# Optimization experiments

Hardware: AMD Instinct MI355X
Metric: run time of the kernel (lower is better)

The kernel has to match this reference:

```python
import jax, jax.numpy as jnp
import numpy as np
import math

LMAX = 3
NCHAN = 32
NEDGE = 50000

# ---------- Wigner 3j (real spherical-harmonic basis), replicating e3nn ----------

def _su2_cg(j1, j2, j3):
    f = math.factorial
    def coeff(m1, m2, m3):
        vmin = int(max(-j1 + j2 + m3, -j1 + m1, 0))
        vmax = int(min(j2 + j3 + m1, j3 - j1 + j2, j3 + m3))
        C = ((2 * j3 + 1) * f(j3 + j1 - j2) * f(j3 - j1 + j2) * f(j1 + j2 - j3) / f(j1 + j2 + j3 + 1)) ** 0.5
        C *= (f(j3 + m3) * f(j3 - m3) * f(j1 - m1) * f(j1 + m1) * f(j2 - m2) * f(j2 + m2)) ** 0.5
        S = 0.0
        for v in range(vmin, vmax + 1):
            S += (-1.0) ** (v + j2 + m2) * f(j2 + j3 + m1 - v) * f(j1 - m1 + v) / (
                f(v) * f(j3 - j1 + j2 - v) * f(j3 + m3 - v) * f(v + j1 - j2 - m3))
        return C * S
    out = np.zeros((2 * j1 + 1, 2 * j2 + 1, 2 * j3 + 1))
    for m1 in range(-j1, j1 + 1):
        for m2 in range(-j2, j2 + 1):
            m3 = m1 + m2
            if -j3 <= m3 <= j3:
                out[m1 + j1, m2 + j2, m3 + j3] = coeff(m1, m2, m3)
    return out

def _q_real_to_complex(l):
    q = np.zeros((2 * l + 1, 2 * l + 1), dtype=np.complex128)
    for m in range(-l, 0):
        q[l + m, l + abs(m)] = 1 / 2 ** 0.5
        q[l + m, l - abs(m)] = -1j / 2 ** 0.5
    q[l, l] = 1.0
    for m in range(1, l + 1):
        q[l + m, l + abs(m)] = (-1) ** m / 2 ** 0.5
        q[l + m, l - abs(m)] = 1j * (-1) ** m / 2 ** 0.5
    return (-1j) ** l * q

def _wigner_3j(l1, l2, l3):
    C = _su2_cg(l1, l2, l3).astype(np.complex128)
    Q1, Q2, Q3 = _q_real_to_complex(l1), _q_real_to_complex(l2), _q_real_to_complex(l3)
    C = np.einsum('ij,kl,mn,ikn->jlm', Q1, Q2, np.conj(Q3.T), C)
    C = np.real(C)
    return C / np.linalg.norm(C)

# ---------- Instruction enumeration (matches the torch module's __init__) ----------

def _build_paths():
    ls = list(range(LMAX + 1))  # irreps 0e,1o,2e,3o -> parity (-1)^l
    ins = []
    for l1 in ls:
        for l2 in ls:
            for l3 in range(abs(l1 - l2), min(l1 + l2, LMAX) + 1):
                if (l1 + l2 + l3) % 2 == 0:  # parity selection p1*p2 == p3
                    ins.append((l1, l2, l3))
    # e3nn Irreps.sort: stable sort of output blocks by ir; pos[i] = sorted position
    order_sorted = sorted(range(len(ins)), key=lambda i: ins[i][2])
    pos = [0] * len(ins)
    for new, old in enumerate(order_sorted):
        pos[old] = new
    # replicate `outputs.insert(ins.i_out, output)` over instruction iteration order
    concat = []
    for idx in range(len(ins)):
        concat.insert(min(pos[idx], len(concat)), idx)
    offs = np.cumsum([0] + [2 * l + 1 for l in ls]).tolist()  # block offsets in dim-16 layout
    # path_weight: component normalization, one path per output block -> sqrt(2*l3+1)
    cg = [jnp.asarray((_wigner_3j(l1, l2, l3) * math.sqrt(2 * l3 + 1)).astype(np.float32))
          for (l1, l2, l3) in ins]
    return ins, pos, concat, offs, cg

_INS, _POS, _CONCAT, _OFFS, _CG = _build_paths()  # 23 instructions, out dim 99


def setup_inputs() -> dict:
    key = jax.random.key(0)
    k1, k2, k3 = jax.random.split(key, 3)
    x = jax.random.normal(k1, (NEDGE, NCHAN, 16), dtype=jnp.float32)
    y = jax.random.normal(k2, (NEDGE, 1, 16), dtype=jnp.float32)
    weights = jax.random.normal(k3, (NEDGE, len(_INS) * NCHAN, 1), dtype=jnp.float32)
    return {"x": x, "y": y, "weights": weights}


def reference(x, y, weights):
    # x: [E, C, 16], y: [E, 1, 16], weights: [E, n_ins*C, 1]
    C = x.shape[1]
    y2 = y[:, 0, :]  # [E, 16]
    outs = [None] * len(_INS)
    for idx, (l1, l2, l3) in enumerate(_INS):
        o1, o2 = _OFFS[l1], _OFFS[l2]
        xb = x[:, :, o1:o1 + 2 * l1 + 1]            # [E, C, 2l1+1]
        yb = y2[:, o2:o2 + 2 * l2 + 1]              # [E, 2l2+1]
        w = weights[:, _POS[idx] * C:(_POS[idx] + 1) * C, 0]  # [E, C]
        # dense CG contraction == sparse gather-multiply-index_add over (mu1,mu2,mu3)
        blk = jnp.einsum('eci,ej,ijk->eck', xb, yb, _CG[idx])  # [E, C, 2l3+1]
        outs[idx] = w[:, :, None] * blk
    return jnp.concatenate([outs[i] for i in _CONCAT], axis=-1)  # [E, C, 99]
```

## Files before the change

kernel.cpp:

```cpp
#include <hip/hip_runtime.h>
#include <math.h>

#define NPATH 23
#define NEDGE 50000
#define NCHAN 32
#define NWROW 736
#define OUTW  99
#define TTOT  439
#define EPB   4
#define NTHR  512
#define NBLK  (NEDGE/EPB)

constexpr int L1[NPATH]    = {0,0,0,0,1,1,1,1,1,1,2,2,2,2,2,2,2,3,3,3,3,3,3};
constexpr int L2[NPATH]    = {0,1,2,3,0,1,1,2,2,3,0,1,1,2,2,3,3,0,1,2,2,3,3};
constexpr int L3[NPATH]    = {0,1,2,3,1,0,2,1,3,2,2,1,3,0,2,1,3,3,2,1,3,0,2};
constexpr int POS[NPATH]   = {0,4,10,17,5,1,11,6,18,12,13,7,19,2,14,8,20,21,15,9,22,3,16};
constexpr int OOFF[NPATH]  = {0,4,7,12,19,1,34,22,39,46,51,31,61,2,73,25,78,85,68,28,92,3,56};
constexpr int TOFF[NPATH]  = {0,1,4,9,16,25,28,43,52,73,88,113,128,163,168,193,208,243,292,327,348,397,404};
constexpr int LOFF[4]      = {0,1,4,9};

#define G0M  0xE0010u
#define G1M  0x700100u
#define G2M  0x7C00u
#define G3LO 0x2Fu
#define G3HI 0x182C0u

typedef _Float16 __attribute__((ext_vector_type(4))) h4;

__device__ __forceinline__ int imx(int a, int b){ return a > b ? a : b; }
__device__ __forceinline__ int imn(int a, int b){ return a < b ? a : b; }

__device__ __forceinline__ double factd(int n){
    double r = 1.0;
    for(int i = 2; i <= n; ++i) r *= (double)i;
    return r;
}

__global__ __launch_bounds__(512) void cg_setup(float* __restrict__ cgd2){
    const int p  = blockIdx.x;
    const int j1 = L1[p], j2 = L2[p], j3 = L3[p];
    const int n1 = 2*j1+1, n2 = 2*j2+1, n3 = 2*j3+1;
    const int o2 = LOFF[j2];
    const int ntot = n1*n2*n3;
    const int t = threadIdx.x;

    __shared__ double scg[343];
    __shared__ double qre[3][49];
    __shared__ double qim[3][49];
    __shared__ double red[512];

    if(t < ntot){
        int a   = t / (n2*n3);
        int rem = t - a*(n2*n3);
        int b   = rem / n3;
        int g   = rem - b*n3;
        int m1 = a - j1, m2 = b - j2, m3 = g - j3;
        double val = 0.0;
        if(m1 + m2 == m3){
            int vmin = imx(imx(-j1 + j2 + m3, -j1 + m1), 0);
            int vmax = imn(imn(j2 + j3 + m1, j3 - j1 + j2), j3 + m3);
            double C = sqrt((2.0*j3 + 1.0) * factd(j3 + j1 - j2) * factd(j3 - j1 + j2)
                            * factd(j1 + j2 - j3) / factd(j1 + j2 + j3 + 1));
            C *= sqrt(factd(j3 + m3) * factd(j3 - m3) * factd(j1 - m1)
                      * factd(j1 + m1) * factd(j2 - m2) * factd(j2 + m2));
            double S = 0.0;
            for(int v = vmin; v <= vmax; ++v){
                double sgn = ((v + j2 + m2) & 1) ? -1.0 : 1.0;
                S += sgn * factd(j2 + j3 + m1 - v) * factd(j1 - m1 + v)
                     / (factd(v) * factd(j3 - j1 + j2 - v) * factd(j3 + m3 - v)
                        * factd(v + j1 - j2 - m3));
            }
            val = C * S;
        }
        scg[t] = val;
    }

    if(t < 3){
        int l = (t == 0) ? j1 : ((t == 1) ? j2 : j3);
        int n = 2*l + 1;
        double* QR = qre[t];
        double* QI = qim[t];
        for(int i = 0; i < 49; ++i){ QR[i] = 0.0; QI[i] = 0.0; }
        const double is2 = 0.70710678118654752440;
        for(int m = -l; m < 0; ++m){
            QR[(l+m)*n + (l-m)] = is2;
            QI[(l+m)*n + (l+m)] = -is2;
        }
        QR[l*n + l] = 1.0;
        for(int m = 1; m <= l; ++m){
            double s = (m & 1) ? -1.0 : 1.0;
            QR[(l+m)*n + (l+m)] = s * is2;
            QI[(l+m)*n + (l-m)] = s * is2;
        }
        double fr, fi;
        switch(l & 3){
            case 0: fr = 1.0;  fi = 0.0;  break;
            case 1: fr = 0.0;  fi = -1.0; break;
            case 2: fr = -1.0; fi = 0.0;  break;
            default: fr = 0.0; fi = 1.0;  break;
        }
        for(int i = 0; i < n*n; ++i){
            double re = QR[i], im = QI[i];
            QR[i] = re*fr - im*fi;
            QI[i] = re*fi + im*fr;
        }
    }
    __syncthreads();

    double val = 0.0;
    if(t < ntot){
        int j   = t / (n2*n3);
        int rem = t - j*(n2*n3);
        int lq  = rem / n3;
        int m   = rem - lq*n3;
        double acc = 0.0;
        for(int i = 0; i < n1; ++i){
            double q1r = qre[0][i*n1 + j], q1i = qim[0][i*n1 + j];
            if(q1r == 0.0 && q1i == 0.0) continue;
            for(int k = 0; k < n2; ++k){
                double q2r = qre[1][k*n2 + lq], q2i = qim[1][k*n2 + lq];
                if(q2r == 0.0 && q2i == 0.0) continue;
                double ar = q1r*q2r - q1i*q2i;
                double ai = q1r*q2i + q1i*q2r;
                for(int n = 0; n < n3; ++n){
                    double cv = scg[(i*n2 + k)*n3 + n];
                    if(cv == 0.0) continue;
                    double q3r = qre[2][n*n3 + m];
                    double q3i = -qim[2][n*n3 + m];
                    acc += cv * (ar*q3r - ai*q3i);
                }
            }
        }
        val = acc;
    }

    red[t] = val * val;
    __syncthreads();
    if(t < 343) scg[t] = val;
    for(int s2 = 256; s2 > 0; s2 >>= 1){
        if(t < s2) red[t] += red[t + s2];
        __syncthreads();
    }
    const double scale = sqrt(2.0*j3 + 1.0) / sqrt(red[0]);

    for(int u = t; u < n1*n3*16; u += 512){
        int sl = u >> 4, jf = u & 15;
        int i  = sl / n3, k = sl - i*n3;
        int j  = jf - o2;
        double v2 = (j >= 0 && j < n2) ? scg[(i*n2 + j)*n3 + k] : 0.0;
        cgd2[(size_t)(TOFF[p] + sl)*16 + jf] = (float)(v2 * scale);
    }
}

template<unsigned MASK>
__device__ __forceinline__ void prefetchW(const float* __restrict__ wbase,
                                          float* __restrict__ wreg)
{
    #pragma unroll
    for(int p = 0; p < NPATH; ++p){
        if((MASK >> p) & 1u)
            wreg[__builtin_popcount(MASK & ((1u << p) - 1u))] = wbase[POS[p]*NCHAN];
    }
}

template<unsigned MASK>
__device__ __forceinline__ void phaseC(const float* __restrict__ xr,
                                       const float* __restrict__ wreg,
                                       const float* __restrict__ Te,
                                       _Float16* __restrict__ ob)
{
    #pragma unroll
    for(int p = 0; p < NPATH; ++p){
        if(!((MASK >> p) & 1u)) continue;
        const int widx = __builtin_popcount(MASK & ((1u << p) - 1u));
        const int n1 = 2*L1[p] + 1;
        const int n3 = 2*L3[p] + 1;
        const int o1 = LOFF[L1[p]];
        const float wp = wreg[widx];
        const float* Tp = Te + TOFF[p];
        #pragma unroll
        for(int k = 0; k < n3; ++k){
            float acc = 0.f;
            #pragma unroll
            for(int i = 0; i < n1; ++i)
                acc = fmaf(xr[o1 + i], Tp[i*n3 + k], acc);
            ob[OOFF[p] + k] = (_Float16)(wp * acc);
        }
    }
}

__global__ __launch_bounds__(NTHR, 8) void tp_main(
    const float* __restrict__ x, const float* __restrict__ y,
    const float* __restrict__ w, const float* __restrict__ cgd2,
    float* __restrict__ out)
{
    __shared__ __align__(16) _Float16 obuf[EPB*NCHAN*OUTW];
    __shared__ float Ts[EPB*TTOT];
    __shared__ float ys[EPB*16];

    const int tid = threadIdx.x;
    const int e0  = blockIdx.x * EPB;

    const int lane = tid & 63;
    const int wid  = tid >> 6;
    const int c    = lane & 31;
    const int grp  = wid & 3;
    const int el   = ((wid >> 2) << 1) | (lane >> 5);
    const int e    = e0 + el;

    const float* wbase = w + (size_t)e*NWROW + c;
    float wreg[5];
    switch(grp){
        case 0: prefetchW<G0M>(wbase, wreg); break;
        case 1: prefetchW<G1M>(wbase, wreg); break;
        case 2: prefetchW<G2M>(wbase, wreg); break;
        default: prefetchW<G3LO>(wbase, wreg); break;
    }

    if(tid < EPB*16) ys[tid] = y[e0*16 + tid];
    __syncthreads();

    const float4* xp = reinterpret_cast<const float4*>(x + (size_t)(e*NCHAN + c)*16);
    float4 x0 = xp[0], x1 = xp[1], x2 = xp[2], x3 = xp[3];

    for(int u = tid; u < EPB*TTOT; u += NTHR){
        int eli = u / TTOT;
        int s   = u - eli*TTOT;
        const float* cr = cgd2 + (size_t)s*16;
        float acc = 0.f;
        #pragma unroll
        for(int j = 0; j < 16; ++j)
            acc = fmaf(ys[eli*16 + j], cr[j], acc);
        Ts[u] = acc;
    }
    __syncthreads();

    float xr[16];
    xr[0]=x0.x;  xr[1]=x0.y;  xr[2]=x0.z;  xr[3]=x0.w;
    xr[4]=x1.x;  xr[5]=x1.y;  xr[6]=x1.z;  xr[7]=x1.w;
    xr[8]=x2.x;  xr[9]=x2.y;  xr[10]=x2.z; xr[11]=x2.w;
    xr[12]=x3.x; xr[13]=x3.y; xr[14]=x3.z; xr[15]=x3.w;

    const float* Te = Ts + el*TTOT;
    _Float16* ob = obuf + el*(NCHAN*OUTW) + c*OUTW;

    switch(grp){
        case 0: phaseC<G0M>(xr, wreg, Te, ob); break;
        case 1: phaseC<G1M>(xr, wreg, Te, ob); break;
        case 2: phaseC<G2M>(xr, wreg, Te, ob); break;
        default: {
            float wregB[5];
            prefetchW<G3HI>(wbase, wregB);
            phaseC<G3LO>(xr, wreg, Te, ob);
            phaseC<G3HI>(xr, wregB, Te, ob);
            break;
        }
    }
    __syncthreads();

    const h4* ob4 = reinterpret_cast<const h4*>(obuf);
    float4* o4 = reinterpret_cast<float4*>(out + (size_t)blockIdx.x * (EPB*NCHAN*OUTW));
    #pragma unroll
    for(int k2 = 0; k2 < 7; ++k2){
        int idx = tid + k2*NTHR;
        if(idx < EPB*NCHAN*OUTW/4){
            h4 hv = ob4[idx];
            float4 fv = { (float)hv[0], (float)hv[1], (float)hv[2], (float)hv[3] };
            o4[idx] = fv;
        }
    }
}

extern "C" void kernel_launch(void* const* d_in, const int* in_sizes, int n_in,
                              void* d_out, int out_size, void* d_ws, size_t ws_size,
                              hipStream_t stream)
{
    const float* x  = (const float*)d_in[0];
    const float* y  = (const float*)d_in[1];
    const float* wt = (const float*)d_in[2];
    float* out = (float*)d_out;
    float* cgd2 = (float*)d_ws;

    cg_setup<<<NPATH, 512, 0, stream>>>(cgd2);
    tp_main<<<NBLK, NTHR, 0, stream>>>(x, y, wt, cgd2, out);
}
```

Before: 251.1 us.

## Split per-edge T-table build into separate kernel and pad rows for vector loads

Pads the per-path CG/T tables so each output row has 4 or 8 entries, which lets the contraction read T with float4 loads. When the workspace is large enough, the per-edge T build moves into its own kernel that writes T to global memory (about 126 MB), and the main kernel streams T from global instead of building it in LDS. Otherwise a fused kernel keeps the LDS path but uses the padded layout. The split path adds a large global write and read of T in exchange for removing the in-block build and its extra barrier.

```diff
diff --git a/kernel.cpp b/kernel.cpp
--- a/kernel.cpp
+++ b/kernel.cpp
@@ -6,10 +6,11 @@
 #define NCHAN 32
 #define NWROW 736
 #define OUTW  99
-#define TTOT  439
 #define EPB   4
 #define NTHR  512
 #define NBLK  (NEDGE/EPB)
+#define TSZ   632
+#define WS_T_OFF 65536
 
 constexpr int L1[NPATH]    = {0,0,0,0,1,1,1,1,1,1,2,2,2,2,2,2,2,3,3,3,3,3,3};
 constexpr int L2[NPATH]    = {0,1,2,3,0,1,1,2,2,3,0,1,1,2,2,3,3,0,1,2,2,3,3};
@@ -19,6 +20,17 @@
 constexpr int TOFF[NPATH]  = {0,1,4,9,16,25,28,43,52,73,88,113,128,163,168,193,208,243,292,327,348,397,404};
 constexpr int LOFF[4]      = {0,1,4,9};
 
+constexpr int PAD(int n1){ return n1 <= 3 ? 4 : 8; }
+struct PT { int v[NPATH]; int total; };
+constexpr PT make_ptoff(){
+    PT t{}; int a = 0;
+    for(int p = 0; p < NPATH; ++p){ t.v[p] = a; a += (2*L3[p]+1)*PAD(2*L1[p]+1); }
+    t.total = a;
+    return t;
+}
+constexpr PT PTOF = make_ptoff();
+static_assert(PTOF.total == TSZ, "padded T size");
+
 #define G0M  0xE0010u
 #define G1M  0x700100u
 #define G2M  0x7C00u
@@ -36,7 +48,7 @@
     return r;
 }
 
-__global__ __launch_bounds__(512) void cg_setup(float* __restrict__ cgd2){
+__global__ __launch_bounds__(512) void cg_setup(float* __restrict__ cgd2p){
     const int p  = blockIdx.x;
     const int j1 = L1[p], j2 = L2[p], j3 = L3[p];
     const int n1 = 2*j1+1, n2 = 2*j2+1, n3 = 2*j3+1;
@@ -143,12 +155,39 @@
     }
     const double scale = sqrt(2.0*j3 + 1.0) / sqrt(red[0]);
 
-    for(int u = t; u < n1*n3*16; u += 512){
-        int sl = u >> 4, jf = u & 15;
-        int i  = sl / n3, k = sl - i*n3;
-        int j  = jf - o2;
-        double v2 = (j >= 0 && j < n2) ? scg[(i*n2 + j)*n3 + k] : 0.0;
-        cgd2[(size_t)(TOFF[p] + sl)*16 + jf] = (float)(v2 * scale);
+    const int padn = PAD(n1);
+    const int sh   = (padn == 8) ? 3 : 2;
+    for(int u = t; u < n3*padn*16; u += 512){
+        int row = u >> 4;
+        int jf  = u & 15;
+        int k   = row >> sh;
+        int ip  = row & (padn - 1);
+        int j   = jf - o2;
+        double v2 = (ip < n1 && j >= 0 && j < n2) ? scg[(ip*n2 + j)*n3 + k] : 0.0;
+        cgd2p[(size_t)(PTOF.v[p] + row)*16 + jf] = (float)(v2 * scale);
+    }
+}
+
+__global__ __launch_bounds__(NTHR) void t_build(
+    const float* __restrict__ y, const float* __restrict__ cgd2p,
+    float* __restrict__ Tbuf)
+{
+    __shared__ float ys[EPB*16];
+    const int tid = threadIdx.x;
+    const int e0  = blockIdx.x * EPB;
+
+    if(tid < EPB*16) ys[tid] = y[e0*16 + tid];
+    __syncthreads();
+
+    for(int u = tid; u < EPB*TSZ; u += NTHR){
+        int eli = u / TSZ;
+        int s   = u - eli*TSZ;
+        const float* cr = cgd2p + (size_t)s*16;
+        float acc = 0.f;
+        #pragma unroll
+        for(int j = 0; j < 16; ++j)
+            acc = fmaf(ys[eli*16 + j], cr[j], acc);
+        Tbuf[(size_t)e0*TSZ + u] = acc;
     }
 }
 
@@ -164,43 +203,51 @@
 }
 
 template<unsigned MASK>
-__device__ __forceinline__ void phaseC(const float* __restrict__ xr,
-                                       const float* __restrict__ wreg,
-                                       const float* __restrict__ Te,
-                                       _Float16* __restrict__ ob)
+__device__ __forceinline__ void phaseCp(const float* __restrict__ xr,
+                                        const float* __restrict__ wreg,
+                                        const float* __restrict__ Te,
+                                        _Float16* __restrict__ ob)
 {
     #pragma unroll
     for(int p = 0; p < NPATH; ++p){
         if(!((MASK >> p) & 1u)) continue;
         const int widx = __builtin_popcount(MASK & ((1u << p) - 1u));
-        const int n1 = 2*L1[p] + 1;
-        const int n3 = 2*L3[p] + 1;
-        const int o1 = LOFF[L1[p]];
+        const int n1  = 2*L1[p] + 1;
+        const int n3  = 2*L3[p] + 1;
+        const int o1  = LOFF[L1[p]];
+        const int pad = PAD(n1);
         const float wp = wreg[widx];
-        const float* Tp = Te + TOFF[p];
         #pragma unroll
         for(int k = 0; k < n3; ++k){
-            float acc = 0.f;
-            #pragma unroll
-            for(int i = 0; i < n1; ++i)
-                acc = fmaf(xr[o1 + i], Tp[i*n3 + k], acc);
-            ob[OOFF[p] + k] = (_Float16)(wp * acc);
-        }
-    }
-}
-
-__global__ __launch_bounds__(NTHR, 8) void tp_main(
-    const float* __restrict__ x, const float* __restrict__ y,
-    const float* __restrict__ w, const float* __restrict__ cgd2,
-    float* __restrict__ out)
+            const float* tr = Te + PTOF.v[p] + k*pad;
+            float4 t0 = *(const float4*)tr;
+            float a = xr[o1] * t0.x;
+            if(n1 > 1){
+                a = fmaf(xr[o1+1], t0.y, a);
+                a = fmaf(xr[o1+2], t0.z, a);
+            }
+            if(n1 > 3){
+                a = fmaf(xr[o1+3], t0.w, a);
+                float4 t1 = *((const float4*)tr + 1);
+                a = fmaf(xr[o1+4], t1.x, a);
+                if(n1 > 5){
+                    a = fmaf(xr[o1+5], t1.y, a);
+                    a = fmaf(xr[o1+6], t1.z, a);
+                }
+            }
+            ob[OOFF[p] + k] = (_Float16)(a * wp);
+        }
+    }
+}
+
+__global__ __launch_bounds__(NTHR, 8) void tp_stream(
+    const float* __restrict__ x, const float* __restrict__ w,
+    const float* __restrict__ Tbuf, float* __restrict__ out)
 {
     __shared__ __align__(16) _Float16 obuf[EPB*NCHAN*OUTW];
-    __shared__ float Ts[EPB*TTOT];
-    __shared__ float ys[EPB*16];
-
-    const int tid = threadIdx.x;
-    const int e0  = blockIdx.x * EPB;
-
+
+    const int tid  = threadIdx.x;
+    const int e0   = blockIdx.x * EPB;
     const int lane = tid & 63;
     const int wid  = tid >> 6;
     const int c    = lane & 31;
@@ -217,23 +264,8 @@
         default: prefetchW<G3LO>(wbase, wreg); break;
     }
 
-    if(tid < EPB*16) ys[tid] = y[e0*16 + tid];
-    __syncthreads();
-
     const float4* xp = reinterpret_cast<const float4*>(x + (size_t)(e*NCHAN + c)*16);
     float4 x0 = xp[0], x1 = xp[1], x2 = xp[2], x3 = xp[3];
-
-    for(int u = tid; u < EPB*TTOT; u += NTHR){
-        int eli = u / TTOT;
-        int s   = u - eli*TTOT;
-        const float* cr = cgd2 + (size_t)s*16;
-        float acc = 0.f;
-        #pragma unroll
-        for(int j = 0; j < 16; ++j)
-            acc = fmaf(ys[eli*16 + j], cr[j], acc);
-        Ts[u] = acc;
-    }
-    __syncthreads();
 
     float xr[16];
     xr[0]=x0.x;  xr[1]=x0.y;  xr[2]=x0.z;  xr[3]=x0.w;
@@ -241,18 +273,18 @@
     xr[8]=x2.x;  xr[9]=x2.y;  xr[10]=x2.z; xr[11]=x2.w;
     xr[12]=x3.x; xr[13]=x3.y; xr[14]=x3.z; xr[15]=x3.w;
 
-    const float* Te = Ts + el*TTOT;
+    const float* Te = Tbuf + (size_t)e*TSZ;
     _Float16* ob = obuf + el*(NCHAN*OUTW) + c*OUTW;
 
     switch(grp){
-        case 0: phaseC<G0M>(xr, wreg, Te, ob); break;
-        case 1: phaseC<G1M>(xr, wreg, Te, ob); break;
-        case 2: phaseC<G2M>(xr, wreg, Te, ob); break;
+        case 0: phaseCp<G0M>(xr, wreg, Te, ob); break;
+        case 1: phaseCp<G1M>(xr, wreg, Te, ob); break;
+        case 2: phaseCp<G2M>(xr, wreg, Te, ob); break;
         default: {
             float wregB[5];
             prefetchW<G3HI>(wbase, wregB);
-            phaseC<G3LO>(xr, wreg, Te, ob);
-            phaseC<G3HI>(xr, wregB, Te, ob);
+            phaseCp<G3LO>(xr, wreg, Te, ob);
+            phaseCp<G3HI>(xr, wregB, Te, ob);
             break;
         }
     }
@@ -271,6 +303,87 @@
     }
 }
 
+__global__ __launch_bounds__(NTHR, 8) void tp_fused(
+    const float* __restrict__ x, const float* __restrict__ y,
+    const float* __restrict__ w, const float* __restrict__ cgd2p,
+    float* __restrict__ out)
+{
+    __shared__ __align__(16) _Float16 obuf[EPB*NCHAN*OUTW];
+    __shared__ float Ts[EPB*TSZ];
+    __shared__ float ys[EPB*16];
+
+    const int tid  = threadIdx.x;
+    const int e0   = blockIdx.x * EPB;
+    const int lane = tid & 63;
+    const int wid  = tid >> 6;
+    const int c    = lane & 31;
+    const int grp  = wid & 3;
+    const int el   = ((wid >> 2) << 1) | (lane >> 5);
+    const int e    = e0 + el;
+
+    const float* wbase = w + (size_t)e*NWROW + c;
+    float wreg[5];
+    switch(grp){
+        case 0: prefetchW<G0M>(wbase, wreg); break;
+        case 1: prefetchW<G1M>(wbase, wreg); break;
+        case 2: prefetchW<G2M>(wbase, wreg); break;
+        default: prefetchW<G3LO>(wbase, wreg); break;
+    }
+
+    if(tid < EPB*16) ys[tid] = y[e0*16 + tid];
+    __syncthreads();
+
+    const float4* xp = reinterpret_cast<const float4*>(x + (size_t)(e*NCHAN + c)*16);
+    float4 x0 = xp[0], x1 = xp[1], x2 = xp[2], x3 = xp[3];
+
+    for(int u = tid; u < EPB*TSZ; u += NTHR){
+        int eli = u / TSZ;
+        int s   = u - eli*TSZ;
+        const float* cr = cgd2p + (size_t)s*16;
+        float acc = 0.f;
+        #pragma unroll
+        for(int j = 0; j < 16; ++j)
+            acc = fmaf(ys[eli*16 + j], cr[j], acc);
+        Ts[u] = acc;
+    }
+    __syncthreads();
+
+    float xr[16];
+    xr[0]=x0.x;  xr[1]=x0.y;  xr[2]=x0.z;  xr[3]=x0.w;
+    xr[4]=x1.x;  xr[5]=x1.y;  xr[6]=x1.z;  xr[7]=x1.w;
+    xr[8]=x2.x;  xr[9]=x2.y;  xr[10]=x2.z; xr[11]=x2.w;
+    xr[12]=x3.x; xr[13]=x3.y; xr[14]=x3.z; xr[15]=x3.w;
+
+    const float* Te = Ts + el*TSZ;
+    _Float16* ob = obuf + el*(NCHAN*OUTW) + c*OUTW;
+
+    switch(grp){
+        case 0: phaseCp<G0M>(xr, wreg, Te, ob); break;
+        case 1: phaseCp<G1M>(xr, wreg, Te, ob); break;
+        case 2: phaseCp<G2M>(xr, wreg, Te, ob); break;
+        default: {
+            float wregB[5];
+            prefetchW<G3HI>(wbase, wregB);
+            phaseCp<G3LO>(xr, wreg, Te, ob);
+            phaseCp<G3HI>(xr, wregB, Te, ob);
+            break;
+        }
+    }
+    __syncthreads();
+
+    const h4* ob4 = reinterpret_cast<const h4*>(obuf);
+    float4* o4 = reinterpret_cast<float4*>(out + (size_t)blockIdx.x * (EPB*NCHAN*OUTW));
+    #pragma unroll
+    for(int k2 = 0; k2 < 7; ++k2){
+        int idx = tid + k2*NTHR;
+        if(idx < EPB*NCHAN*OUTW/4){
+            h4 hv = ob4[idx];
+            float4 fv = { (float)hv[0], (float)hv[1], (float)hv[2], (float)hv[3] };
+            o4[idx] = fv;
+        }
+    }
+}
+
 extern "C" void kernel_launch(void* const* d_in, const int* in_sizes, int n_in,
                               void* d_out, int out_size, void* d_ws, size_t ws_size,
                               hipStream_t stream)
@@ -279,8 +392,16 @@
     const float* y  = (const float*)d_in[1];
     const float* wt = (const float*)d_in[2];
     float* out = (float*)d_out;
-    float* cgd2 = (float*)d_ws;
-
-    cg_setup<<<NPATH, 512, 0, stream>>>(cgd2);
-    tp_main<<<NBLK, NTHR, 0, stream>>>(x, y, wt, cgd2, out);
-}
+    float* cgd2p = (float*)d_ws;
+
+    const size_t needed = (size_t)WS_T_OFF + (size_t)NEDGE*TSZ*sizeof(float);
+
+    cg_setup<<<NPATH, 512, 0, stream>>>(cgd2p);
+    if(ws_size >= needed){
+        float* Tbuf = (float*)((char*)d_ws + WS_T_OFF);
+        t_build<<<NBLK, NTHR, 0, stream>>>(y, cgd2p, Tbuf);
+        tp_stream<<<NBLK, NTHR, 0, stream>>>(x, wt, Tbuf, out);
+    } else {
+        tp_fused<<<NBLK, NTHR, 0, stream>>>(x, y, wt, cgd2p, out);
+    }
+}
```

After: 539.4 us. 115% more time.
